# Performance work log

Measured on AMD Instinct MI355X. Metric: run time of the kernel, lower is better.

## Reference

```python
import jax, jax.numpy as jnp
import numpy as np

BATCH, SEQ, L_IN, M_ENC, H_DIM, F_MLP = 16, 2048, 256, 512, 1024, 4096
LN_EPS = 1e-5


def setup_inputs() -> dict:
    key = jax.random.key(0)
    ks = jax.random.split(key, 13)
    x = jax.random.normal(ks[0], (BATCH, SEQ, L_IN), dtype=jnp.float32)
    W_enc = jax.random.normal(ks[1], (L_IN, M_ENC), dtype=jnp.float32) / np.sqrt(L_IN)
    b_enc = jnp.zeros((M_ENC,), dtype=jnp.float32)
    W_B = jax.random.normal(ks[2], (M_ENC, H_DIM), dtype=jnp.float32) / np.sqrt(M_ENC)
    # fixed reservoir matrix, scaled for spectral radius < 1
    A = jax.random.normal(ks[3], (H_DIM, H_DIM), dtype=jnp.float32) * (0.99 / np.sqrt(H_DIM))
    W_res = jax.random.normal(ks[4], (L_IN, H_DIM), dtype=jnp.float32) / np.sqrt(L_IN)
    b_res = jnp.zeros((H_DIM,), dtype=jnp.float32)
    ln_g = jnp.ones((H_DIM,), dtype=jnp.float32)
    ln_b = jnp.zeros((H_DIM,), dtype=jnp.float32)
    W1 = jax.random.normal(ks[5], (H_DIM, F_MLP), dtype=jnp.float32) / np.sqrt(H_DIM)
    b1 = jnp.zeros((F_MLP,), dtype=jnp.float32)
    W2 = jax.random.normal(ks[6], (F_MLP, H_DIM), dtype=jnp.float32) / np.sqrt(F_MLP)
    b2 = jnp.zeros((H_DIM,), dtype=jnp.float32)
    return {"x": x, "W_enc": W_enc, "b_enc": b_enc, "W_B": W_B, "A": A,
            "W_res": W_res, "b_res": b_res, "ln_g": ln_g, "ln_b": ln_b,
            "W1": W1, "b1": b1, "W2": W2, "b2": b2}


def reference(x, W_enc, b_enc, W_B, A, W_res, b_res, ln_g, ln_b, W1, b1, W2, b2):
    # encoder + B applied to all timesteps at once: [B,S,H]
    Bu = (jnp.einsum('bsl,lm->bsm', x, W_enc) + b_enc) @ W_B
    # linear recurrence h_t = h_{t-1} @ A + Bu_t, h_0 = Bu_0 (zeros init works)
    Bu_t = jnp.swapaxes(Bu, 0, 1)  # [S,B,H]

    def step(h, bu):
        h = h @ A + bu
        return h, h

    h0 = jnp.zeros((x.shape[0], A.shape[0]), dtype=x.dtype)
    _, Hs = jax.lax.scan(step, h0, Bu_t)
    H_seq_pre = jnp.swapaxes(Hs, 0, 1)  # [B,S,H]

    residual = jnp.einsum('bsl,lh->bsh', x, W_res) + b_res
    z = H_seq_pre + residual
    mu = jnp.mean(z, axis=-1, keepdims=True)
    var = jnp.var(z, axis=-1, keepdims=True)
    H_seq = (z - mu) * jax.lax.rsqrt(var + LN_EPS) * ln_g + ln_b

    h_last = H_seq[:, -1, :]
    out = jax.nn.relu(h_last @ W1 + b1) @ W2 + b2
    return out, H_seq_pre
```

## Files before the change

### kernel.cpp

```cpp
#include <hip/hip_runtime.h>
#include <math.h>

#define BATCH 16
#define SEQ   2048
#define L_INP 256
#define MENC  512
#define HD    1024
#define FM    4096
#define TCH   16
#define NCH   128
#define NROW  (BATCH*NCH)

typedef unsigned short u16;
typedef __attribute__((ext_vector_type(8))) short s8v;
typedef __attribute__((ext_vector_type(4))) float f4v;

__device__ inline u16 bf16_rne(float x) {
    unsigned u = __builtin_bit_cast(unsigned, x);
    u += 0x7fff + ((u >> 16) & 1);
    return (u16)(u >> 16);
}
__device__ inline float bf16_tof(u16 h) {
    unsigned u = ((unsigned)h) << 16;
    return __builtin_bit_cast(float, u);
}
__device__ inline void split2(float x, u16& h, u16& l) {
    h = bf16_rne(x);
    l = bf16_rne(x - bf16_tof(h));
}

__device__ inline void gload_lds16(const u16* g, u16* l) {
    __builtin_amdgcn_global_load_lds(
        (const __attribute__((address_space(1))) void*)g,
        (__attribute__((address_space(3))) void*)l, 16, 0, 0);
}

#define TS 64
#define KT 16
#define LP 68
__device__ inline float4 add4(float4 a, float4 b) {
    return make_float4(a.x + b.x, a.y + b.y, a.z + b.z, a.w + b.w);
}
template<int MODE>
__global__ __launch_bounds__(256)
void gemm_k(const float* __restrict__ IN, const float* __restrict__ W,
            float* __restrict__ OUT, const float* __restrict__ BIAS,
            int M, int N, int K, int ldIN)
{
    __shared__ float As[KT][LP];
    __shared__ float Bs[KT][LP];
    const int tid  = threadIdx.x;
    const int tx   = tid & 15, ty = tid >> 4;
    const int col0 = blockIdx.x * TS;
    const int row0 = blockIdx.y * TS;
    const int la_k = tid & 15, la_r = tid >> 4;
    const int lb_j = tid & 63, lb_k = tid >> 6;
    float acc[4][4] = {};

    for (int k0 = 0; k0 < K; k0 += KT) {
        #pragma unroll
        for (int i = 0; i < 4; ++i) {
            int r = la_r + (i << 4);
            int grow = row0 + r;
            float v = 0.f;
            if (grow < M) v = IN[(long)grow * ldIN + k0 + la_k];
            As[la_k][r] = v;
        }
        #pragma unroll
        for (int i = 0; i < 4; ++i) {
            int k = lb_k + (i << 2);
            Bs[k][lb_j] = W[(long)(k0 + k) * N + col0 + lb_j];
        }
        __syncthreads();
        #pragma unroll
        for (int kk = 0; kk < KT; ++kk) {
            float4 av = *(const float4*)&As[kk][ty << 2];
            float4 bv = *(const float4*)&Bs[kk][tx << 2];
            float ar[4] = {av.x, av.y, av.z, av.w};
            float br[4] = {bv.x, bv.y, bv.z, bv.w};
            #pragma unroll
            for (int i = 0; i < 4; ++i)
                #pragma unroll
                for (int j = 0; j < 4; ++j)
                    acc[i][j] = fmaf(ar[i], br[j], acc[i][j]);
        }
        __syncthreads();
    }
    const int jc = col0 + (tx << 2);
    float4 bias4 = make_float4(0.f, 0.f, 0.f, 0.f);
    if constexpr (MODE == 1 || MODE == 2) bias4 = *(const float4*)&BIAS[jc];
    #pragma unroll
    for (int i = 0; i < 4; ++i) {
        int row = row0 + (ty << 2) + i;
        if (row >= M) continue;
        float4 vv = make_float4(acc[i][0], acc[i][1], acc[i][2], acc[i][3]);
        if constexpr (MODE == 1 || MODE == 2) vv = add4(vv, bias4);
        if constexpr (MODE == 2) {
            vv.x = fmaxf(vv.x, 0.f); vv.y = fmaxf(vv.y, 0.f);
            vv.z = fmaxf(vv.z, 0.f); vv.w = fmaxf(vv.w, 0.f);
        }
        *(float4*)&OUT[(long)row * N + jc] = vv;
    }
}

template<int KC>
__global__ __launch_bounds__(256)
void skgemm(const float* __restrict__ IN, const float* __restrict__ W,
            float* __restrict__ PART, int M, int N, int ldIN)
{
    const int tid = threadIdx.x;
    const int m   = tid >> 4;
    const int cq  = tid & 15;
    const int col = blockIdx.x * 64 + cq * 4;
    const int p   = blockIdx.y;
    const int k0  = p * KC;
    __shared__ float sIN[16 * KC];
    #pragma unroll
    for (int i = tid; i < 16 * KC; i += 256) {
        int mm = i / KC, kk = i - mm * KC;
        sIN[i] = (mm < M) ? IN[(long)mm * ldIN + k0 + kk] : 0.f;
    }
    __syncthreads();
    float4 acc = make_float4(0.f, 0.f, 0.f, 0.f);
    const float* wp = W + (long)k0 * N + col;
    #pragma unroll 4
    for (int k = 0; k < KC; ++k) {
        float a = sIN[m * KC + k];
        float4 w4 = *(const float4*)&wp[(long)k * N];
        acc.x = fmaf(a, w4.x, acc.x);
        acc.y = fmaf(a, w4.y, acc.y);
        acc.z = fmaf(a, w4.z, acc.z);
        acc.w = fmaf(a, w4.w, acc.w);
    }
    *(float4*)&PART[((long)p * 16 + m) * N + col] = acc;
}

template<int MODE>
__global__ __launch_bounds__(256)
void skred(const float* __restrict__ PART, const float* __restrict__ BIAS,
           float* __restrict__ OUT, int M, int N, int P)
{
    long i = (long)blockIdx.x * 256 + threadIdx.x;
    if (i >= (long)M * N) return;
    int mm = (int)(i / N), n = (int)(i - (long)mm * N);
    float s = 0.f;
    for (int p = 0; p < P; ++p) s += PART[((long)p * 16 + mm) * N + n];
    if constexpr (MODE == 1 || MODE == 2) s += BIAS[n];
    if constexpr (MODE == 2) s = fmaxf(s, 0.f);
    OUT[(long)mm * N + n] = s;
}

#define LK 32
template<int MODE, int KDIM, int BT>
__global__ __launch_bounds__(256)
void pgemm(const u16* __restrict__ INh, const u16* __restrict__ INl,
           const u16* __restrict__ Wh,  const u16* __restrict__ Wl,
           float* __restrict__ HOUT,
           const u16* __restrict__ EXh, const u16* __restrict__ EXl,
           u16* __restrict__ Oh, u16* __restrict__ Ol,
           u16* __restrict__ OTh, u16* __restrict__ OTl,
           const float* __restrict__ BIAS,
           int t, int dshift, int inslot, int oslot)
{
    constexpr int MT  = BT / 32;
    constexpr int NG  = BT / 64;
    const int tid = threadIdx.x;
    const int z = blockIdx.z;
    if constexpr (MODE == 0) {
        long oin = ((long)(inslot + z)) << 20;
        INh += oin; INl += oin;
        long oo = ((long)(oslot + z)) << 20;
        Oh += oo; Ol += oo; OTh += oo; OTl += oo;
    }
    if constexpr (MODE == 3) {
        long ow = ((long)z) << 20;
        Wh += ow; Wl += ow;
    }
    const int row0 = blockIdx.y * BT;
    const int col0 = blockIdx.x * BT;

    __shared__ u16 sAh[BT * LK], sAl[BT * LK], sBh[BT * LK], sBl[BT * LK];

    const int lane = tid & 63;
    const int wv   = tid >> 6;
    const int wrow = (wv >> 1) * (BT / 2);
    const int wcol = (wv & 1) * (BT / 2);
    const int fl   = lane & 15;
    const int quad = lane >> 4;

    const int srow = lane >> 2;
    const int sq   = lane & 3;
    const int qsw  = sq ^ ((lane >> 3) & 3);
    long offA[NG], offB[NG];
    int  lbs[NG];
    #pragma unroll
    for (int h = 0; h < NG; ++h) {
        int rin = h * 64 + wv * 16 + srow;
        int gA = row0 + rin;
        if constexpr (MODE == 2 || MODE == 3) { gA -= dshift; if (gA < 0) gA = 0; }
        offA[h] = (long)gA * KDIM + qsw * 8;
        offB[h] = (long)(col0 + rin) * KDIM + qsw * 8;
        lbs[h]  = (h * 64 + wv * 16) * LK;
    }

    const int fsw = (quad ^ ((fl >> 1) & 3)) << 3;

    bool dead[MT] = {};
    if constexpr (MODE == 2 || MODE == 3) {
        #pragma unroll
        for (int mt = 0; mt < MT; ++mt)
            dead[mt] = (row0 + wrow + mt * 16 + fl) < dshift;
    }

    f4v acc[MT][MT] = {};
    const s8v zer = {0, 0, 0, 0, 0, 0, 0, 0};

    for (int k0 = 0; k0 < KDIM; k0 += 32) {
        __syncthreads();
        #pragma unroll
        for (int h = 0; h < NG; ++h) {
            gload_lds16(INh + offA[h] + k0, &sAh[lbs[h]]);
            gload_lds16(INl + offA[h] + k0, &sAl[lbs[h]]);
            gload_lds16(Wh  + offB[h] + k0, &sBh[lbs[h]]);
            gload_lds16(Wl  + offB[h] + k0, &sBl[lbs[h]]);
        }
        __syncthreads();
        s8v ah[MT], al[MT], bh[MT], bl[MT];
        #pragma unroll
        for (int mt = 0; mt < MT; ++mt) {
            int off = (wrow + mt * 16 + fl) * LK + fsw;
            ah[mt] = *(const s8v*)&sAh[off];
            al[mt] = *(const s8v*)&sAl[off];
            if constexpr (MODE == 2 || MODE == 3) {
                if (dead[mt]) { ah[mt] = zer; al[mt] = zer; }
            }
        }
        #pragma unroll
        for (int nt = 0; nt < MT; ++nt) {
            int off = (wcol + nt * 16 + fl) * LK + fsw;
            bh[nt] = *(const s8v*)&sBh[off];
            bl[nt] = *(const s8v*)&sBl[off];
        }
        #pragma unroll
        for (int mt = 0; mt < MT; ++mt)
            #pragma unroll
            for (int nt = 0; nt < MT; ++nt) {
                acc[mt][nt] = __builtin_amdgcn_mfma_f32_16x16x32_bf16(ah[mt], bh[nt], acc[mt][nt], 0, 0, 0);
                acc[mt][nt] = __builtin_amdgcn_mfma_f32_16x16x32_bf16(ah[mt], bl[nt], acc[mt][nt], 0, 0, 0);
                acc[mt][nt] = __builtin_amdgcn_mfma_f32_16x16x32_bf16(al[mt], bh[nt], acc[mt][nt], 0, 0, 0);
            }
    }

    #pragma unroll
    for (int mt = 0; mt < MT; ++mt) {
        #pragma unroll
        for (int nt = 0; nt < MT; ++nt) {
            #pragma unroll
            for (int reg = 0; reg < 4; ++reg) {
                int grow = row0 + wrow + mt * 16 + quad * 4 + reg;
                int gcol = col0 + wcol + nt * 16 + fl;
                float v = acc[mt][nt][reg];
                if constexpr (MODE == 0) {
                    u16 h, l; split2(v, h, l);
                    long o  = ((long)grow << 10) + gcol;
                    long ot = ((long)gcol << 10) + grow;
                    Oh[o] = h; Ol[o] = l;
                    OTh[ot] = h; OTl[ot] = l;
                } else if constexpr (MODE == 1) {
                    int b = grow & 15, c = grow >> 4;
                    long exoff = ((long)(b * SEQ + c * TCH + t) << 10) + gcol;
                    v += HOUT[exoff];
                    HOUT[exoff] = v;
                    long o = ((long)grow << 10) + gcol;
                    u16 h, l; split2(v, h, l);
                    Oh[o] = h; Ol[o] = l;
                } else if constexpr (MODE == 2) {
                    long o = ((long)grow << 10) + gcol;
                    v += bf16_tof(EXh[o]) + bf16_tof(EXl[o]);
                    u16 h, l; split2(v, h, l);
                    Oh[o] = h; Ol[o] = l;
                } else if constexpr (MODE == 3) {
                    if (grow >= 16) {
                        int b = grow & 15, c = grow >> 4;
                        long exoff = ((long)(b * SEQ + c * TCH + z) << 10) + gcol;
                        HOUT[exoff] += v;
                    }
                } else {
                    v += BIAS[gcol];
                    HOUT[((long)grow << 10) + gcol] = v;
                    if ((grow & 15) == 0) {
                        int b = grow >> 11;
                        int s = grow & (SEQ - 1);
                        long so = ((long)(s + b) << 10) + gcol;
                        u16 h, l; split2(v, h, l);
                        Oh[so] = h; Ol[so] = l;
                    }
                }
            }
        }
    }
}

__global__ __launch_bounds__(256)
void splitA_k(const float* __restrict__ A, u16* __restrict__ nH, u16* __restrict__ nL,
              u16* __restrict__ tH, u16* __restrict__ tL)
{
    __shared__ unsigned sm[64][65];
    const int r0 = blockIdx.y * 64, c0 = blockIdx.x * 64;
    const int tr = threadIdx.x >> 4;
    const int tc = (threadIdx.x & 15) * 4;
    #pragma unroll
    for (int i = 0; i < 4; ++i) {
        int row = tr + i * 16;
        float4 v = *(const float4*)&A[((long)(r0 + row) << 10) + c0 + tc];
        float vv[4] = {v.x, v.y, v.z, v.w};
        u16 h[4], l[4];
        #pragma unroll
        for (int j = 0; j < 4; ++j) {
            split2(vv[j], h[j], l[j]);
            sm[row][tc + j] = (((unsigned)h[j]) << 16) | l[j];
        }
        long o = ((long)(r0 + row) << 10) + c0 + tc;
        *(uint2*)&nH[o] = make_uint2((unsigned)h[0] | ((unsigned)h[1] << 16),
                                     (unsigned)h[2] | ((unsigned)h[3] << 16));
        *(uint2*)&nL[o] = make_uint2((unsigned)l[0] | ((unsigned)l[1] << 16),
                                     (unsigned)l[2] | ((unsigned)l[3] << 16));
    }
    __syncthreads();
    #pragma unroll
    for (int i = 0; i < 4; ++i) {
        int n = tr + i * 16;
        unsigned p[4];
        #pragma unroll
        for (int j = 0; j < 4; ++j) p[j] = sm[tc + j][n];
        long o = ((long)(c0 + n) << 10) + r0 + tc;
        *(uint2*)&tH[o] = make_uint2((p[0] >> 16) | (p[1] & 0xffff0000u),
                                     (p[2] >> 16) | (p[3] & 0xffff0000u));
        *(uint2*)&tL[o] = make_uint2((p[0] & 0xffffu) | (p[1] << 16),
                                     (p[2] & 0xffffu) | (p[3] << 16));
    }
}

__global__ __launch_bounds__(256)
void splitX_k(const float* __restrict__ X, u16* __restrict__ xh, u16* __restrict__ xl)
{
    long i4 = (long)blockIdx.x * 256 + threadIdx.x;
    long base = i4 * 4;
    float4 v = *(const float4*)&X[base];
    float vv[4] = {v.x, v.y, v.z, v.w};
    u16 h[4], l[4];
    #pragma unroll
    for (int j = 0; j < 4; ++j) split2(vv[j], h[j], l[j]);
    *(uint2*)&xh[base] = make_uint2((unsigned)h[0] | ((unsigned)h[1] << 16),
                                    (unsigned)h[2] | ((unsigned)h[3] << 16));
    *(uint2*)&xl[base] = make_uint2((unsigned)l[0] | ((unsigned)l[1] << 16),
                                    (unsigned)l[2] | ((unsigned)l[3] << 16));
}

__global__ __launch_bounds__(256)
void splitWt_k(const float* __restrict__ Wf, u16* __restrict__ th, u16* __restrict__ tl)
{
    int i = blockIdx.x * 256 + threadIdx.x;
    int n = i >> 8, k = i & 255;
    float v = Wf[((long)k << 10) + n];
    u16 h, l; split2(v, h, l);
    th[i] = h; tl[i] = l;
}

__global__ __launch_bounds__(256)
void ln_k(const u16* __restrict__ Sh, const u16* __restrict__ Sl,
          const float* __restrict__ Rlast,
          const float* __restrict__ g, const float* __restrict__ bta,
          float* __restrict__ zout)
{
    __shared__ double red[256];
    int b = blockIdx.x, tid = threadIdx.x;
    long base = ((long)((NCH - 1) * BATCH + b)) << 10;
    const float* rr = Rlast + b * HD;
    double s = 0.0;
    for (int j = tid; j < HD; j += 256)
        s += (double)(bf16_tof(Sh[base + j]) + bf16_tof(Sl[base + j])) + (double)rr[j];
    red[tid] = s; __syncthreads();
    for (int o = 128; o > 0; o >>= 1) { if (tid < o) red[tid] += red[tid + o]; __syncthreads(); }
    double mu = red[0] * (1.0 / HD);
    __syncthreads();
    double ss = 0.0;
    for (int j = tid; j < HD; j += 256) {
        double zz = (double)(bf16_tof(Sh[base + j]) + bf16_tof(Sl[base + j])) + (double)rr[j] - mu;
        ss += zz * zz;
    }
    red[tid] = ss; __syncthreads();
    for (int o = 128; o > 0; o >>= 1) { if (tid < o) red[tid] += red[tid + o]; __syncthreads(); }
    double inv = 1.0 / sqrt(red[0] * (1.0 / HD) + 1e-5);
    __syncthreads();
    for (int j = tid; j < HD; j += 256) {
        double zz = (double)(bf16_tof(Sh[base + j]) + bf16_tof(Sl[base + j])) + (double)rr[j];
        zout[b * HD + j] = (float)(((zz - mu) * inv) * (double)g[j] + (double)bta[j]);
    }
}

extern "C" void kernel_launch(void* const* d_in, const int* in_sizes, int n_in,
                              void* d_out, int out_size, void* d_ws, size_t ws_size,
                              hipStream_t stream)
{
    const float* x     = (const float*)d_in[0];
    const float* W_enc = (const float*)d_in[1];
    const float* b_enc = (const float*)d_in[2];
    const float* W_B   = (const float*)d_in[3];
    const float* A     = (const float*)d_in[4];
    const float* W_res = (const float*)d_in[5];
    const float* b_res = (const float*)d_in[6];
    const float* ln_g  = (const float*)d_in[7];
    const float* ln_b  = (const float*)d_in[8];
    const float* W1    = (const float*)d_in[9];
    const float* b1    = (const float*)d_in[10];
    const float* W2    = (const float*)d_in[11];
    const float* b2    = (const float*)d_in[12];

    float* out0 = (float*)d_out;
    float* Hout = out0 + (long)BATCH * HD;

    char* p = (char*)d_ws;
    auto alloc = [&](size_t bytes) { void* r = (void*)p; p += (bytes + 255) & ~(size_t)255; return r; };
    const long M2 = 1L << 20;
    u16* natH = (u16*)alloc(22 * M2 * 2);
    u16* natL = (u16*)alloc(22 * M2 * 2);
    u16* trH  = (u16*)alloc(22 * M2 * 2);
    u16* trL  = (u16*)alloc(22 * M2 * 2);
    const long SB = (long)NROW * HD;
    u16* SPh[3]; u16* SPl[3];
    for (int i = 0; i < 3; ++i) { SPh[i] = (u16*)alloc(SB * 2); SPl[i] = (u16*)alloc(SB * 2); }
    float* Wf    = (float*)alloc((long)L_INP * HD * 4);
    float* bf    = (float*)alloc(HD * 4);
    float* Rlast = (float*)alloc(BATCH * HD * 4);
    float* zln   = (float*)alloc(BATCH * HD * 4);
    float* t1    = (float*)alloc((long)BATCH * FM * 4);
    float* PART  = (float*)alloc(32L * 16 * 4096 * 4);

    const long MS = (long)BATCH * SEQ;
    u16* xh  = natH;
    u16* xl  = natH + MS * L_INP;
    u16* wth = trH;
    u16* wtl = trH + (long)HD * L_INP;

    dim3 blk(256);

    gemm_k<0><<<dim3(HD / TS, L_INP / TS), blk, 0, stream>>>(W_enc, W_B, Wf, nullptr, L_INP, HD, MENC, MENC);
    skgemm<128><<<dim3(HD / 64, MENC / 128), blk, 0, stream>>>(b_enc, W_B, PART, 1, HD, MENC);
    skred<0><<<dim3((HD + 255) / 256), blk, 0, stream>>>(PART, nullptr, bf, 1, HD, MENC / 128);
    splitWt_k<<<dim3((HD * L_INP) / 256), blk, 0, stream>>>(Wf, wth, wtl);
    splitX_k<<<dim3((int)(MS * L_INP / 4 / 256)), blk, 0, stream>>>(x, xh, xl);
    pgemm<4, L_INP, 128><<<dim3(HD / 128, (int)(MS / 128)), blk, 0, stream>>>(
        xh, xl, wth, wtl, Hout, nullptr, nullptr,
        SPh[0], SPl[0], nullptr, nullptr, bf, 0, 0, 0, 0);

    splitA_k<<<dim3(16, 16), blk, 0, stream>>>(A, natH, natL, trH, trL);

    pgemm<0, HD, 64><<<dim3(16, 16, 1), blk, 0, stream>>>(natH, natL, trH, trL, nullptr, nullptr, nullptr,
                                                          natH, natL, trH, trL, nullptr, 0, 0, 0, 1);
    pgemm<0, HD, 64><<<dim3(16, 16, 2), blk, 0, stream>>>(natH, natL, trH + (1L << 20), trL + (1L << 20), nullptr, nullptr, nullptr,
                                                          natH, natL, trH, trL, nullptr, 0, 0, 0, 2);
    pgemm<0, HD, 128><<<dim3(8, 8, 4), blk, 0, stream>>>(natH, natL, trH + (3L << 20), trL + (3L << 20), nullptr, nullptr, nullptr,
                                                         natH, natL, trH, trL, nullptr, 0, 0, 0, 4);
    pgemm<0, HD, 128><<<dim3(8, 8, 8), blk, 0, stream>>>(natH, natL, trH + (7L << 20), trL + (7L << 20), nullptr, nullptr, nullptr,
                                                         natH, natL, trH, trL, nullptr, 0, 0, 0, 8);
    for (int i = 0; i < 6; ++i) {
        int src = 15 + i;
        pgemm<0, HD, 64><<<dim3(16, 16, 1), blk, 0, stream>>>(natH, natL, trH + ((long)src << 20), trL + ((long)src << 20),
                                                              nullptr, nullptr, nullptr,
                                                              natH, natL, trH, trL, nullptr, 0, 0, src, src + 1);
    }

    int cur = 0, nxt = 1;
    for (int t = 1; t < TCH; ++t) {
        pgemm<1, HD, 64><<<dim3(16, 32), blk, 0, stream>>>(SPh[cur], SPl[cur], trH, trL, Hout, nullptr, nullptr,
                                                           SPh[nxt], SPl[nxt], nullptr, nullptr, nullptr, t, 0, 0, 0);
        int tmp = cur; cur = nxt; nxt = tmp;
    }

    int pin = cur;
    int tgt[2] = { nxt, 2 };
    for (int i = 0; i < 7; ++i) {
        int d = (1 << i) * BATCH;
        int wslot = (i == 0) ? 15 : (16 + i - 1);
        int ob = tgt[i & 1];
        pgemm<2, HD, 64><<<dim3(16, 32), blk, 0, stream>>>(SPh[pin], SPl[pin],
                                                           trH + ((long)wslot << 20), trL + ((long)wslot << 20),
                                                           nullptr, SPh[pin], SPl[pin],
                                                           SPh[ob], SPl[ob], nullptr, nullptr, nullptr, 0, d, 0, 0);
        pin = ob;
    }
    int Sfin = pin;

    pgemm<3, HD, 128><<<dim3(8, 16, TCH), blk, 0, stream>>>(SPh[Sfin], SPl[Sfin], trH, trL, Hout, nullptr, nullptr,
                                                            nullptr, nullptr, nullptr, nullptr, nullptr, 0, BATCH, 0, 0);

    skgemm<64><<<dim3(HD / 64, L_INP / 64), blk, 0, stream>>>(x + (long)(SEQ - 1) * L_INP, W_res, PART, BATCH, HD, SEQ * L_INP);
    skred<1><<<dim3((BATCH * HD + 255) / 256), blk, 0, stream>>>(PART, b_res, Rlast, BATCH, HD, L_INP / 64);
    ln_k<<<dim3(BATCH), blk, 0, stream>>>(SPh[Sfin], SPl[Sfin], Rlast, ln_g, ln_b, zln);
    skgemm<128><<<dim3(FM / 64, HD / 128), blk, 0, stream>>>(zln, W1, PART, BATCH, FM, HD);
    skred<2><<<dim3((BATCH * FM + 255) / 256), blk, 0, stream>>>(PART, b1, t1, BATCH, FM, HD / 128);
    skgemm<128><<<dim3(HD / 64, FM / 128), blk, 0, stream>>>(t1, W2, PART, BATCH, HD, FM);
    skred<1><<<dim3((BATCH * HD + 255) / 256), blk, 0, stream>>>(PART, b2, out0, BATCH, HD, FM / 128);
}
```

Baseline: 1.550 ms.

## Split-K the single power-matrix GEMMs, swizzle block order, skip dead row tiles

The 1024x1024 matrix-power GEMMs that ran as a lone 256-block grid now split the K dimension four ways (new MODE 5) to fill more CUs. A new reduction kernel sums the four partials and writes the bf16 hi/lo split in both natural and transposed layouts. The block index is also remapped across groups of eight for locality, and MODE 2 blocks whose rows lie entirely below the shift skip the K loop. This costs extra partial-sum traffic and one more launch per power step. It also reuses an SP buffer as scratch, which must not alias live data.

```diff
diff --git a/kernel.cpp b/kernel.cpp
--- a/kernel.cpp
+++ b/kernel.cpp
@@ -165,7 +165,17 @@
     constexpr int MT  = BT / 32;
     constexpr int NG  = BT / 64;
     const int tid = threadIdx.x;
-    const int z = blockIdx.z;
+
+    const int gx = gridDim.x, gy = gridDim.y;
+    const int nwg = gx * gy * gridDim.z;
+    const int fid = blockIdx.x + gx * (blockIdx.y + gy * blockIdx.z);
+    const int cpx = nwg >> 3;
+    const int swz = (fid & 7) * cpx + (fid >> 3);
+    const int bx  = swz % gx;
+    const int rm_ = swz / gx;
+    const int by  = rm_ % gy;
+    const int z   = rm_ / gy;
+
     if constexpr (MODE == 0) {
         long oin = ((long)(inslot + z)) << 20;
         INh += oin; INl += oin;
@@ -176,8 +186,8 @@
         long ow = ((long)z) << 20;
         Wh += ow; Wl += ow;
     }
-    const int row0 = blockIdx.y * BT;
-    const int col0 = blockIdx.x * BT;
+    const int row0 = by * BT;
+    const int col0 = bx * BT;
 
     __shared__ u16 sAh[BT * LK], sAl[BT * LK], sBh[BT * LK], sBl[BT * LK];
 
@@ -215,7 +225,16 @@
     f4v acc[MT][MT] = {};
     const s8v zer = {0, 0, 0, 0, 0, 0, 0, 0};
 
-    for (int k0 = 0; k0 < KDIM; k0 += 32) {
+    int kbeg = 0, kend = KDIM;
+    if constexpr (MODE == 5) {
+        const int kch = KDIM / gridDim.z;
+        kbeg = z * kch; kend = kbeg + kch;
+    }
+    bool skipK = false;
+    if constexpr (MODE == 2) skipK = (row0 + BT <= dshift);
+
+    if (!skipK)
+    for (int k0 = kbeg; k0 < kend; k0 += 32) {
         __syncthreads();
         #pragma unroll
         for (int h = 0; h < NG; ++h) {
@@ -285,7 +304,7 @@
                         long exoff = ((long)(b * SEQ + c * TCH + z) << 10) + gcol;
                         HOUT[exoff] += v;
                     }
-                } else {
+                } else if constexpr (MODE == 4) {
                     v += BIAS[gcol];
                     HOUT[((long)grow << 10) + gcol] = v;
                     if ((grow & 15) == 0) {
@@ -295,9 +314,54 @@
                         u16 h, l; split2(v, h, l);
                         Oh[so] = h; Ol[so] = l;
                     }
+                } else {
+                    HOUT[((long)z << 20) + ((long)grow << 10) + gcol] = v;
                 }
             }
         }
+    }
+}
+
+__global__ __launch_bounds__(256)
+void powred_k(const float* __restrict__ PART, int P,
+              u16* __restrict__ nH, u16* __restrict__ nL,
+              u16* __restrict__ tH, u16* __restrict__ tL)
+{
+    __shared__ unsigned sm[64][65];
+    const int r0 = blockIdx.y * 64, c0 = blockIdx.x * 64;
+    const int tr = threadIdx.x >> 4;
+    const int tc = (threadIdx.x & 15) * 4;
+    #pragma unroll
+    for (int i = 0; i < 4; ++i) {
+        int row = tr + i * 16;
+        float4 v = make_float4(0.f, 0.f, 0.f, 0.f);
+        for (int p = 0; p < P; ++p)
+            v = add4(v, *(const float4*)&PART[((long)p << 20) + ((long)(r0 + row) << 10) + c0 + tc]);
+        float vv[4] = {v.x, v.y, v.z, v.w};
+        u16 h[4], l[4];
+        #pragma unroll
+        for (int j = 0; j < 4; ++j) {
+            split2(vv[j], h[j], l[j]);
+            sm[row][tc + j] = (((unsigned)h[j]) << 16) | l[j];
+        }
+        long o = ((long)(r0 + row) << 10) + c0 + tc;
+        *(uint2*)&nH[o] = make_uint2((unsigned)h[0] | ((unsigned)h[1] << 16),
+                                     (unsigned)h[2] | ((unsigned)h[3] << 16));
+        *(uint2*)&nL[o] = make_uint2((unsigned)l[0] | ((unsigned)l[1] << 16),
+                                     (unsigned)l[2] | ((unsigned)l[3] << 16));
+    }
+    __syncthreads();
+    #pragma unroll
+    for (int i = 0; i < 4; ++i) {
+        int n = tr + i * 16;
+        unsigned p[4];
+        #pragma unroll
+        for (int j = 0; j < 4; ++j) p[j] = sm[tc + j][n];
+        long o = ((long)(c0 + n) << 10) + r0 + tc;
+        *(uint2*)&tH[o] = make_uint2((p[0] >> 16) | (p[1] & 0xffff0000u),
+                                     (p[2] >> 16) | (p[3] & 0xffff0000u));
+        *(uint2*)&tL[o] = make_uint2((p[0] & 0xffffu) | (p[1] << 16),
+                                     (p[2] & 0xffffu) | (p[3] << 16));
     }
 }
 
@@ -442,6 +506,7 @@
     u16* xl  = natH + MS * L_INP;
     u16* wth = trH;
     u16* wtl = trH + (long)HD * L_INP;
+    float* PWP = (float*)SPh[1];
 
     dim3 blk(256);
 
@@ -456,8 +521,11 @@
 
     splitA_k<<<dim3(16, 16), blk, 0, stream>>>(A, natH, natL, trH, trL);
 
-    pgemm<0, HD, 64><<<dim3(16, 16, 1), blk, 0, stream>>>(natH, natL, trH, trL, nullptr, nullptr, nullptr,
-                                                          natH, natL, trH, trL, nullptr, 0, 0, 0, 1);
+    pgemm<5, HD, 64><<<dim3(16, 16, 4), blk, 0, stream>>>(natH, natL, trH, trL, PWP,
+                                                          nullptr, nullptr, nullptr, nullptr,
+                                                          nullptr, nullptr, nullptr, 0, 0, 0, 0);
+    powred_k<<<dim3(16, 16), blk, 0, stream>>>(PWP, 4, natH + (1L << 20), natL + (1L << 20),
+                                               trH + (1L << 20), trL + (1L << 20));
     pgemm<0, HD, 64><<<dim3(16, 16, 2), blk, 0, stream>>>(natH, natL, trH + (1L << 20), trL + (1L << 20), nullptr, nullptr, nullptr,
                                                           natH, natL, trH, trL, nullptr, 0, 0, 0, 2);
     pgemm<0, HD, 128><<<dim3(8, 8, 4), blk, 0, stream>>>(natH, natL, trH + (3L << 20), trL + (3L << 20), nullptr, nullptr, nullptr,
@@ -465,10 +533,13 @@
     pgemm<0, HD, 128><<<dim3(8, 8, 8), blk, 0, stream>>>(natH, natL, trH + (7L << 20), trL + (7L << 20), nullptr, nullptr, nullptr,
                                                          natH, natL, trH, trL, nullptr, 0, 0, 0, 8);
     for (int i = 0; i < 6; ++i) {
-        int src = 15 + i;
-        pgemm<0, HD, 64><<<dim3(16, 16, 1), blk, 0, stream>>>(natH, natL, trH + ((long)src << 20), trL + ((long)src << 20),
-                                                              nullptr, nullptr, nullptr,
-                                                              natH, natL, trH, trL, nullptr, 0, 0, src, src + 1);
+        long src = 15 + i;
+        pgemm<5, HD, 64><<<dim3(16, 16, 4), blk, 0, stream>>>(natH + (src << 20), natL + (src << 20),
+                                                              trH + (src << 20), trL + (src << 20), PWP,
+                                                              nullptr, nullptr, nullptr, nullptr,
+                                                              nullptr, nullptr, nullptr, 0, 0, 0, 0);
+        powred_k<<<dim3(16, 16), blk, 0, stream>>>(PWP, 4, natH + ((src + 1) << 20), natL + ((src + 1) << 20),
+                                                   trH + ((src + 1) << 20), trL + ((src + 1) << 20));
     }
 
     int cur = 0, nxt = 1;
```

New measurement: 1.602 ms. 1.03x slower.

## Fuse chunk scan and doubling steps into one cooperative kernel with grid sync

Applied to the files above, without the earlier changes.

The 15 sequential chunk-recurrence GEMM launches and the 7 log-doubling carry-propagation launches are replaced by a single cooperative kernel. It runs the same 64x64 split-bf16 MFMA tiles and uses grid.sync between steps. Tiles whose rows are entirely below the doubling shift skip the GEMM and only copy their input. The pgemm kernel also gains an XCD-aware swizzle of its block index to improve L2 locality. The aim is to remove per-launch gaps on the serial critical path, at the cost of grid-wide barriers and a 512-block grid that must stay co-resident.

```diff
diff --git a/kernel.cpp b/kernel.cpp
--- a/kernel.cpp
+++ b/kernel.cpp
@@ -1,5 +1,8 @@
 #include <hip/hip_runtime.h>
+#include <hip/hip_cooperative_groups.h>
 #include <math.h>
+
+namespace cg = cooperative_groups;
 
 #define BATCH 16
 #define SEQ   2048
@@ -156,16 +159,25 @@
 void pgemm(const u16* __restrict__ INh, const u16* __restrict__ INl,
            const u16* __restrict__ Wh,  const u16* __restrict__ Wl,
            float* __restrict__ HOUT,
-           const u16* __restrict__ EXh, const u16* __restrict__ EXl,
            u16* __restrict__ Oh, u16* __restrict__ Ol,
            u16* __restrict__ OTh, u16* __restrict__ OTl,
            const float* __restrict__ BIAS,
-           int t, int dshift, int inslot, int oslot)
+           int dshift, int inslot, int oslot)
 {
     constexpr int MT  = BT / 32;
     constexpr int NG  = BT / 64;
     const int tid = threadIdx.x;
-    const int z = blockIdx.z;
+
+    const int gx = gridDim.x, gy = gridDim.y;
+    const int nwg = gx * gy * gridDim.z;
+    const int fid = blockIdx.x + gx * (blockIdx.y + gy * blockIdx.z);
+    const int cpx = nwg >> 3;
+    const int swz = (fid & 7) * cpx + (fid >> 3);
+    const int bx  = swz % gx;
+    const int rm_ = swz / gx;
+    const int by  = rm_ % gy;
+    const int z   = rm_ / gy;
+
     if constexpr (MODE == 0) {
         long oin = ((long)(inslot + z)) << 20;
         INh += oin; INl += oin;
@@ -176,8 +188,8 @@
         long ow = ((long)z) << 20;
         Wh += ow; Wl += ow;
     }
-    const int row0 = blockIdx.y * BT;
-    const int col0 = blockIdx.x * BT;
+    const int row0 = by * BT;
+    const int col0 = bx * BT;
 
     __shared__ u16 sAh[BT * LK], sAl[BT * LK], sBh[BT * LK], sBl[BT * LK];
 
@@ -197,7 +209,7 @@
     for (int h = 0; h < NG; ++h) {
         int rin = h * 64 + wv * 16 + srow;
         int gA = row0 + rin;
-        if constexpr (MODE == 2 || MODE == 3) { gA -= dshift; if (gA < 0) gA = 0; }
+        if constexpr (MODE == 3) { gA -= dshift; if (gA < 0) gA = 0; }
         offA[h] = (long)gA * KDIM + qsw * 8;
         offB[h] = (long)(col0 + rin) * KDIM + qsw * 8;
         lbs[h]  = (h * 64 + wv * 16) * LK;
@@ -206,7 +218,7 @@
     const int fsw = (quad ^ ((fl >> 1) & 3)) << 3;
 
     bool dead[MT] = {};
-    if constexpr (MODE == 2 || MODE == 3) {
+    if constexpr (MODE == 3) {
         #pragma unroll
         for (int mt = 0; mt < MT; ++mt)
             dead[mt] = (row0 + wrow + mt * 16 + fl) < dshift;
@@ -231,7 +243,7 @@
             int off = (wrow + mt * 16 + fl) * LK + fsw;
             ah[mt] = *(const s8v*)&sAh[off];
             al[mt] = *(const s8v*)&sAl[off];
-            if constexpr (MODE == 2 || MODE == 3) {
+            if constexpr (MODE == 3) {
                 if (dead[mt]) { ah[mt] = zer; al[mt] = zer; }
             }
         }
@@ -266,19 +278,6 @@
                     long ot = ((long)gcol << 10) + grow;
                     Oh[o] = h; Ol[o] = l;
                     OTh[ot] = h; OTl[ot] = l;
-                } else if constexpr (MODE == 1) {
-                    int b = grow & 15, c = grow >> 4;
-                    long exoff = ((long)(b * SEQ + c * TCH + t) << 10) + gcol;
-                    v += HOUT[exoff];
-                    HOUT[exoff] = v;
-                    long o = ((long)grow << 10) + gcol;
-                    u16 h, l; split2(v, h, l);
-                    Oh[o] = h; Ol[o] = l;
-                } else if constexpr (MODE == 2) {
-                    long o = ((long)grow << 10) + gcol;
-                    v += bf16_tof(EXh[o]) + bf16_tof(EXl[o]);
-                    u16 h, l; split2(v, h, l);
-                    Oh[o] = h; Ol[o] = l;
                 } else if constexpr (MODE == 3) {
                     if (grow >= 16) {
                         int b = grow & 15, c = grow >> 4;
@@ -301,6 +300,135 @@
     }
 }
 
+__device__ __forceinline__ void tile64(const u16* __restrict__ INh, const u16* __restrict__ INl,
+    const u16* __restrict__ Wh, const u16* __restrict__ Wl,
+    u16* sAh, u16* sAl, u16* sBh, u16* sBl,
+    int row0, int col0, int dshift, int tid, f4v (&acc)[2][2])
+{
+    const int lane = tid & 63, wv = tid >> 6;
+    const int wrow = (wv >> 1) << 5, wcol = (wv & 1) << 5;
+    const int fl = lane & 15, quad = lane >> 4;
+    const int srow = lane >> 2, sq = lane & 3;
+    const int qsw = sq ^ ((lane >> 3) & 3);
+    const int rin = wv * 16 + srow;
+    int gA = row0 + rin - dshift; if (gA < 0) gA = 0;
+    const long offA = ((long)gA << 10) + qsw * 8;
+    const long offB = ((long)(col0 + rin) << 10) + qsw * 8;
+    const int lb  = (wv * 16) * LK;
+    const int fsw = (quad ^ ((fl >> 1) & 3)) << 3;
+    bool dead[2];
+    dead[0] = (row0 + wrow + fl) < dshift;
+    dead[1] = (row0 + wrow + 16 + fl) < dshift;
+    const s8v zer = {0, 0, 0, 0, 0, 0, 0, 0};
+    for (int k0 = 0; k0 < 1024; k0 += 32) {
+        __syncthreads();
+        gload_lds16(INh + offA + k0, &sAh[lb]);
+        gload_lds16(INl + offA + k0, &sAl[lb]);
+        gload_lds16(Wh  + offB + k0, &sBh[lb]);
+        gload_lds16(Wl  + offB + k0, &sBl[lb]);
+        __syncthreads();
+        s8v ah[2], al[2], bh[2], bl[2];
+        #pragma unroll
+        for (int mt = 0; mt < 2; ++mt) {
+            int off = (wrow + mt * 16 + fl) * LK + fsw;
+            ah[mt] = *(const s8v*)&sAh[off];
+            al[mt] = *(const s8v*)&sAl[off];
+            if (dead[mt]) { ah[mt] = zer; al[mt] = zer; }
+        }
+        #pragma unroll
+        for (int nt = 0; nt < 2; ++nt) {
+            int off = (wcol + nt * 16 + fl) * LK + fsw;
+            bh[nt] = *(const s8v*)&sBh[off];
+            bl[nt] = *(const s8v*)&sBl[off];
+        }
+        #pragma unroll
+        for (int mt = 0; mt < 2; ++mt)
+            #pragma unroll
+            for (int nt = 0; nt < 2; ++nt) {
+                acc[mt][nt] = __builtin_amdgcn_mfma_f32_16x16x32_bf16(ah[mt], bh[nt], acc[mt][nt], 0, 0, 0);
+                acc[mt][nt] = __builtin_amdgcn_mfma_f32_16x16x32_bf16(ah[mt], bl[nt], acc[mt][nt], 0, 0, 0);
+                acc[mt][nt] = __builtin_amdgcn_mfma_f32_16x16x32_bf16(al[mt], bh[nt], acc[mt][nt], 0, 0, 0);
+            }
+    }
+}
+
+__global__ __launch_bounds__(256, 2)
+void scan_coop(u16* S0h, u16* S0l, u16* S1h, u16* S1l, u16* S2h, u16* S2l,
+               const u16* __restrict__ trH, const u16* __restrict__ trL,
+               float* __restrict__ HOUT)
+{
+    __shared__ u16 sAh[64 * LK], sAl[64 * LK], sBh[64 * LK], sBl[64 * LK];
+    u16* SH[3] = {S0h, S1h, S2h};
+    u16* SL[3] = {S0l, S1l, S2l};
+    const int tid  = threadIdx.x;
+    const int row0 = blockIdx.y * 64;
+    const int col0 = blockIdx.x * 64;
+    const int lane = tid & 63, wv = tid >> 6;
+    const int wrow = (wv >> 1) << 5, wcol = (wv & 1) << 5;
+    const int fl = lane & 15, quad = lane >> 4;
+    cg::grid_group grid = cg::this_grid();
+
+    for (int t = 1; t < TCH; ++t) {
+        const u16* ih = SH[(t - 1) & 1];
+        const u16* il = SL[(t - 1) & 1];
+        u16* oh = SH[t & 1];
+        u16* ol = SL[t & 1];
+        f4v acc[2][2] = {};
+        tile64(ih, il, trH, trL, sAh, sAl, sBh, sBl, row0, col0, 0, tid, acc);
+        #pragma unroll
+        for (int mt = 0; mt < 2; ++mt)
+            #pragma unroll
+            for (int nt = 0; nt < 2; ++nt)
+                #pragma unroll
+                for (int reg = 0; reg < 4; ++reg) {
+                    int grow = row0 + wrow + mt * 16 + quad * 4 + reg;
+                    int gcol = col0 + wcol + nt * 16 + fl;
+                    float v = acc[mt][nt][reg];
+                    int b = grow & 15, c = grow >> 4;
+                    long exoff = ((long)(b * SEQ + c * TCH + t) << 10) + gcol;
+                    v += HOUT[exoff];
+                    HOUT[exoff] = v;
+                    long o = ((long)grow << 10) + gcol;
+                    u16 h, l; split2(v, h, l);
+                    oh[o] = h; ol[o] = l;
+                }
+        __threadfence();
+        grid.sync();
+    }
+
+    int pin = 1;
+    for (int i = 0; i < 7; ++i) {
+        int d = (1 << i) * BATCH;
+        long wslot = (i == 0) ? 15 : (15 + i);
+        int ob = (i & 1) ? 2 : 0;
+        const u16* ih = SH[pin];
+        const u16* il = SL[pin];
+        u16* oh = SH[ob];
+        u16* ol = SL[ob];
+        f4v acc[2][2] = {};
+        bool skip = (row0 + 64 <= d);
+        if (!skip)
+            tile64(ih, il, trH + (wslot << 20), trL + (wslot << 20),
+                   sAh, sAl, sBh, sBl, row0, col0, d, tid, acc);
+        #pragma unroll
+        for (int mt = 0; mt < 2; ++mt)
+            #pragma unroll
+            for (int nt = 0; nt < 2; ++nt)
+                #pragma unroll
+                for (int reg = 0; reg < 4; ++reg) {
+                    int grow = row0 + wrow + mt * 16 + quad * 4 + reg;
+                    int gcol = col0 + wcol + nt * 16 + fl;
+                    long o = ((long)grow << 10) + gcol;
+                    float v = acc[mt][nt][reg] + bf16_tof(ih[o]) + bf16_tof(il[o]);
+                    u16 h, l; split2(v, h, l);
+                    oh[o] = h; ol[o] = l;
+                }
+        __threadfence();
+        grid.sync();
+        pin = ob;
+    }
+}
+
 __global__ __launch_bounds__(256)
 void splitA_k(const float* __restrict__ A, u16* __restrict__ nH, u16* __restrict__ nL,
               u16* __restrict__ tH, u16* __restrict__ tL)
@@ -451,49 +579,37 @@
     splitWt_k<<<dim3((HD * L_INP) / 256), blk, 0, stream>>>(Wf, wth, wtl);
     splitX_k<<<dim3((int)(MS * L_INP / 4 / 256)), blk, 0, stream>>>(x, xh, xl);
     pgemm<4, L_INP, 128><<<dim3(HD / 128, (int)(MS / 128)), blk, 0, stream>>>(
-        xh, xl, wth, wtl, Hout, nullptr, nullptr,
-        SPh[0], SPl[0], nullptr, nullptr, bf, 0, 0, 0, 0);
+        xh, xl, wth, wtl, Hout,
+        SPh[0], SPl[0], nullptr, nullptr, bf, 0, 0, 0);
 
     splitA_k<<<dim3(16, 16), blk, 0, stream>>>(A, natH, natL, trH, trL);
 
-    pgemm<0, HD, 64><<<dim3(16, 16, 1), blk, 0, stream>>>(natH, natL, trH, trL, nullptr, nullptr, nullptr,
-                                                          natH, natL, trH, trL, nullptr, 0, 0, 0, 1);
-    pgemm<0, HD, 64><<<dim3(16, 16, 2), blk, 0, stream>>>(natH, natL, trH + (1L << 20), trL + (1L << 20), nullptr, nullptr, nullptr,
-                                                          natH, natL, trH, trL, nullptr, 0, 0, 0, 2);
-    pgemm<0, HD, 128><<<dim3(8, 8, 4), blk, 0, stream>>>(natH, natL, trH + (3L << 20), trL + (3L << 20), nullptr, nullptr, nullptr,
-                                                         natH, natL, trH, trL, nullptr, 0, 0, 0, 4);
-    pgemm<0, HD, 128><<<dim3(8, 8, 8), blk, 0, stream>>>(natH, natL, trH + (7L << 20), trL + (7L << 20), nullptr, nullptr, nullptr,
-                                                         natH, natL, trH, trL, nullptr, 0, 0, 0, 8);
+    pgemm<0, HD, 64><<<dim3(16, 16, 1), blk, 0, stream>>>(natH, natL, trH, trL, nullptr,
+                                                          natH, natL, trH, trL, nullptr, 0, 0, 1);
+    pgemm<0, HD, 64><<<dim3(16, 16, 2), blk, 0, stream>>>(natH, natL, trH + (1L << 20), trL + (1L << 20), nullptr,
+                                                          natH, natL, trH, trL, nullptr, 0, 0, 2);
+    pgemm<0, HD, 128><<<dim3(8, 8, 4), blk, 0, stream>>>(natH, natL, trH + (3L << 20), trL + (3L << 20), nullptr,
+                                                         natH, natL, trH, trL, nullptr, 0, 0, 4);
+    pgemm<0, HD, 128><<<dim3(8, 8, 8), blk, 0, stream>>>(natH, natL, trH + (7L << 20), trL + (7L << 20), nullptr,
+                                                         natH, natL, trH, trL, nullptr, 0, 0, 8);
     for (int i = 0; i < 6; ++i) {
         int src = 15 + i;
         pgemm<0, HD, 64><<<dim3(16, 16, 1), blk, 0, stream>>>(natH, natL, trH + ((long)src << 20), trL + ((long)src << 20),
-                                                              nullptr, nullptr, nullptr,
-                                                              natH, natL, trH, trL, nullptr, 0, 0, src, src + 1);
-    }
-
-    int cur = 0, nxt = 1;
-    for (int t = 1; t < TCH; ++t) {
-        pgemm<1, HD, 64><<<dim3(16, 32), blk, 0, stream>>>(SPh[cur], SPl[cur], trH, trL, Hout, nullptr, nullptr,
-                                                           SPh[nxt], SPl[nxt], nullptr, nullptr, nullptr, t, 0, 0, 0);
-        int tmp = cur; cur = nxt; nxt = tmp;
-    }
-
-    int pin = cur;
-    int tgt[2] = { nxt, 2 };
-    for (int i = 0; i < 7; ++i) {
-        int d = (1 << i) * BATCH;
-        int wslot = (i == 0) ? 15 : (16 + i - 1);
-        int ob = tgt[i & 1];
-        pgemm<2, HD, 64><<<dim3(16, 32), blk, 0, stream>>>(SPh[pin], SPl[pin],
-                                                           trH + ((long)wslot << 20), trL + ((long)wslot << 20),
-                                                           nullptr, SPh[pin], SPl[pin],
-                                                           SPh[ob], SPl[ob], nullptr, nullptr, nullptr, 0, d, 0, 0);
-        pin = ob;
-    }
-    int Sfin = pin;
-
-    pgemm<3, HD, 128><<<dim3(8, 16, TCH), blk, 0, stream>>>(SPh[Sfin], SPl[Sfin], trH, trL, Hout, nullptr, nullptr,
-                                                            nullptr, nullptr, nullptr, nullptr, nullptr, 0, BATCH, 0, 0);
+                                                              nullptr,
+                                                              natH, natL, trH, trL, nullptr, 0, src, src + 1);
+    }
+
+    {
+        u16 *a0 = SPh[0], *b0 = SPl[0], *a1 = SPh[1], *b1_ = SPl[1], *a2 = SPh[2], *b2_ = SPl[2];
+        const u16 *wh = trH, *wl = trL;
+        float* ho = Hout;
+        void* kargs[] = {&a0, &b0, &a1, &b1_, &a2, &b2_, &wh, &wl, &ho};
+        hipLaunchCooperativeKernel((void*)scan_coop, dim3(16, 32), dim3(256), kargs, 0, stream);
+    }
+    int Sfin = 0;
+
+    pgemm<3, HD, 128><<<dim3(8, 16, TCH), blk, 0, stream>>>(SPh[Sfin], SPl[Sfin], trH, trL, Hout,
+                                                            nullptr, nullptr, nullptr, nullptr, nullptr, BATCH, 0, 0);
 
     skgemm<64><<<dim3(HD / 64, L_INP / 64), blk, 0, stream>>>(x + (long)(SEQ - 1) * L_INP, W_res, PART, BATCH, HD, SEQ * L_INP);
     skred<1><<<dim3((BATCH * HD + 255) / 256), blk, 0, stream>>>(PART, b_res, Rlast, BATCH, HD, L_INP / 64);
```

Result: slower. 4.148 ms (+167.6%).
